# Kernel tuning notes

Measured on AMD Instinct MI355X. Metric: run time of the kernel, lower is better.

The kernel has to match this reference:

```python
import jax, jax.numpy as jnp
import numpy as np

PAD = 0
C_CONST = 0.1712209


def setup_inputs() -> dict:
    key = jax.random.key(0)
    ks = jax.random.split(key, 6)
    tlen, bsz, slen, hsize, vocab = 64, 32, 64, 1024, 32000
    hidden = jax.random.normal(ks[0], (tlen, bsz, hsize), dtype=jnp.float32)
    context = jax.random.normal(ks[1], (slen, bsz, hsize), dtype=jnp.float32)
    src = jax.random.randint(ks[2], (bsz, slen), 0, vocab, dtype=jnp.int64)
    stdv = 1.0 / np.sqrt(hsize)
    W_gen = jax.random.uniform(ks[3], (vocab, hsize), dtype=jnp.float32, minval=-stdv, maxval=stdv)
    b_gen = jnp.zeros((vocab,), dtype=jnp.float32)
    # Xavier-like init for the copy gate
    w_copy = jax.random.normal(ks[4], (hsize,), dtype=jnp.float32) * np.sqrt(2.0 / (hsize + 1))
    b_copy = jnp.zeros((1,), dtype=jnp.float32)
    return {"hidden": hidden, "context": context, "src": src,
            "W_gen": W_gen, "b_gen": b_gen, "w_copy": w_copy, "b_copy": b_copy}


def reference(hidden, context, src, W_gen, b_gen, w_copy, b_copy):
    tlen, bsz, hsize = hidden.shape
    # p(z=1): probability of copying, [tlen, bsz, 1]
    copy_prob = jax.nn.sigmoid(jnp.einsum('tbh,h->tb', hidden, w_copy) + b_copy[0])[..., None]
    # generator distribution over tgt vocab
    logits = jnp.einsum('tbh,vh->tbv', hidden, W_gen) + b_gen
    prob = jax.nn.softmax(logits.astype(jnp.float32), axis=-1)
    p_g = prob * (1.0 - copy_prob)  # [tlen, bsz, vocab]
    # copy attention over source positions: bmm(query[b,t,h], keys[b,s,h]^T)
    attn_score = jnp.einsum('tbh,sbh->bts', hidden, context)  # [bsz, tlen, slen]
    src_mask = (src == PAD)[:, None, :]  # [bsz, 1, slen]
    attn_score = jnp.where(src_mask, -jnp.inf, attn_score.astype(jnp.float32))
    attns = jax.nn.softmax(attn_score, axis=-1)  # [bsz, tlen, slen]
    p_c = jnp.transpose(attns, (1, 0, 2)) * copy_prob  # [tlen, bsz, slen]
    # scatter_add copy probs into vocab distribution along dim 2
    slen = src.shape[1]
    idx_src = jnp.broadcast_to(src[None, :, :], (tlen, bsz, slen))
    t_idx = jnp.arange(tlen)[:, None, None]
    b_idx = jnp.arange(bsz)[None, :, None]
    p_g = p_g.at[t_idx, b_idx, idx_src].add(p_c)
    return jnp.log(p_g) + C_CONST
```

## Files before the change

kernel.cpp:

```cpp
#include <hip/hip_runtime.h>
#include <hip/hip_bf16.h>
#include <stdint.h>

#define TLEN 64
#define BSZ 32
#define SLEN 64
#define HS 1024
#define VOC 32000
#define NROW (TLEN*BSZ)
#define C_CONST_F 0.1712209f
#define BK 64

typedef __attribute__((ext_vector_type(8))) short short8;
typedef __attribute__((ext_vector_type(4))) float f32x4;

static __device__ __forceinline__ ushort f2bf(float f) {
    uint32_t u = __builtin_bit_cast(uint32_t, f);
    uint32_t r = (u + 0x7fffu + ((u >> 16) & 1u)) >> 16;
    return (ushort)r;
}
static __device__ __forceinline__ float bf2f(ushort u) {
    uint32_t v = ((uint32_t)u) << 16;
    return __builtin_bit_cast(float, v);
}
static __device__ __forceinline__ void async16(const void* g, void* lds) {
    __builtin_amdgcn_global_load_lds(
        (const __attribute__((address_space(1))) void*)g,
        (__attribute__((address_space(3))) void*)lds, 16, 0, 0);
}
static __device__ __forceinline__ int swz12(int e) { return e ^ (((e >> 4) & 15) << 1); }

__global__ __launch_bounds__(256) void gate_kernel(const float* __restrict__ hidden,
                                                   const float* __restrict__ w_copy,
                                                   const float* __restrict__ b_copy,
                                                   float* __restrict__ cp) {
    int wid = threadIdx.x >> 6, lane = threadIdx.x & 63;
    int row = blockIdx.x * 4 + wid;
    const float* h = hidden + (size_t)row * HS;
    float acc = 0.f;
    for (int i = 0; i < 4; ++i) {
        int off = (i * 64 + lane) * 4;
        float4 a = *(const float4*)(h + off);
        float4 w = *(const float4*)(w_copy + off);
        acc += a.x * w.x + a.y * w.y + a.z * w.z + a.w * w.w;
    }
    for (int m = 32; m >= 1; m >>= 1) acc += __shfl_xor(acc, m, 64);
    if (lane == 0) cp[row] = 1.f / (1.f + expf(-(acc + b_copy[0])));
}

__global__ __launch_bounds__(256) void attn_kernel(const float* __restrict__ hidden,
                                                   const float* __restrict__ context,
                                                   const int* __restrict__ src,
                                                   const float* __restrict__ cp,
                                                   float* __restrict__ p_c) {
    int row = blockIdx.x;
    int b = row & (BSZ - 1);
    int tid = threadIdx.x, wid = tid >> 6, lane = tid & 63;
    __shared__ float hrow[HS];
    __shared__ float sc[SLEN];
    *(float4*)(hrow + tid * 4) = *(const float4*)(hidden + (size_t)row * HS + tid * 4);
    __syncthreads();
    for (int j = 0; j < 16; ++j) {
        int s = wid * 16 + j;
        const float* c = context + ((size_t)s * BSZ + b) * HS;
        float acc = 0.f;
        for (int i = 0; i < 4; ++i) {
            int off = (i * 64 + lane) * 4;
            float4 cv = *(const float4*)(c + off);
            float4 hv = *(const float4*)(hrow + off);
            acc += cv.x * hv.x + cv.y * hv.y + cv.z * hv.z + cv.w * hv.w;
        }
        for (int m = 32; m >= 1; m >>= 1) acc += __shfl_xor(acc, m, 64);
        if (lane == 0) sc[s] = acc;
    }
    __syncthreads();
    if (tid < SLEN) {
        float v = sc[tid];
        if (src[b * SLEN + tid] == 0) v = -INFINITY;
        float m = v;
        for (int k = 32; k >= 1; k >>= 1) m = fmaxf(m, __shfl_xor(m, k, 64));
        float e = expf(v - m);
        float ssum = e;
        for (int k = 32; k >= 1; k >>= 1) ssum += __shfl_xor(ssum, k, 64);
        p_c[row * SLEN + tid] = (e / ssum) * cp[row];
    }
}

__global__ __launch_bounds__(256) void cvt_kernel(const float* __restrict__ in,
                                                  ushort* __restrict__ out, int n4) {
    int i = blockIdx.x * blockDim.x + threadIdx.x;
    if (i >= n4) return;
    float4 v = ((const float4*)in)[i];
    ushort4 o;
    o.x = f2bf(v.x); o.y = f2bf(v.y); o.z = f2bf(v.z); o.w = f2bf(v.w);
    ((ushort4*)out)[i] = o;
}

template <bool BF16L>
__global__ __launch_bounds__(256) void gemm_kernel(const ushort* __restrict__ A,
                                                   const ushort* __restrict__ B,
                                                   const float* __restrict__ b_gen,
                                                   void* __restrict__ logits,
                                                   float* __restrict__ partials ) {
    __shared__ ushort sAB[2 * 128 * BK];
    ushort* sA = sAB;
    ushort* sB = sAB + 128 * BK;

    int orig = blockIdx.x;
    int wg = (orig & 7) * 500 + (orig >> 3);
    int mIdx = wg & 15;
    int nIdx = wg >> 4;
    int m0 = mIdx * 128, n0 = nIdx * 128;
    int tid = threadIdx.x, wid = tid >> 6, lane = tid & 63;
    int wm = (wid >> 1) * 64, wn = (wid & 1) * 64;
    int lr = lane & 15, lg = lane >> 4;

    const ushort* gaP[4]; const ushort* gbP[4]; char* laP[4]; char* lbP[4];
    for (int j = 0; j < 4; ++j) {
        int slot = j * 256 + tid;
        int row = slot >> 3;
        int cc = (slot & 7) ^ (row & 7);
        gaP[j] = A + (size_t)(m0 + row) * HS + cc * 8;
        gbP[j] = B + (size_t)(n0 + row) * HS + cc * 8;
        laP[j] = (char*)sA + (size_t)(j * 256 + wid * 64) * 16;
        lbP[j] = (char*)sB + (size_t)(j * 256 + wid * 64) * 16;
    }

    f32x4 acc[4][4];
    for (int m = 0; m < 4; ++m)
        for (int n = 0; n < 4; ++n)
            acc[m][n] = f32x4{0.f, 0.f, 0.f, 0.f};

    int offA[4][2], offB[4][2];
    for (int mb = 0; mb < 4; ++mb) {
        int row = wm + mb * 16 + lr;
        for (int kk = 0; kk < 2; ++kk)
            offA[mb][kk] = row * (BK * 2) + (((kk * 4 + lg) ^ (row & 7)) << 4);
    }
    for (int nb = 0; nb < 4; ++nb) {
        int row = wn + nb * 16 + lr;
        for (int kk = 0; kk < 2; ++kk)
            offB[nb][kk] = row * (BK * 2) + (((kk * 4 + lg) ^ (row & 7)) << 4);
    }

    for (int k0 = 0; k0 < HS; k0 += BK) {
        for (int j = 0; j < 4; ++j) {
            async16(gaP[j] + k0, laP[j]);
            async16(gbP[j] + k0, lbP[j]);
        }
        __syncthreads();
        for (int kk = 0; kk < 2; ++kk) {
            short8 af[4], bfr[4];
            for (int mb = 0; mb < 4; ++mb)
                af[mb] = *(const short8*)((const char*)sA + offA[mb][kk]);
            for (int nb = 0; nb < 4; ++nb)
                bfr[nb] = *(const short8*)((const char*)sB + offB[nb][kk]);
            for (int mb = 0; mb < 4; ++mb)
                for (int nb = 0; nb < 4; ++nb)
                    acc[mb][nb] = __builtin_amdgcn_mfma_f32_16x16x32_bf16(af[mb], bfr[nb], acc[mb][nb], 0, 0, 0);
        }
        __syncthreads();
    }

    float bg[4];
    for (int nb = 0; nb < 4; ++nb) bg[nb] = b_gen[n0 + wn + nb * 16 + lr];
    int chunk = nIdx * 2 + (wid & 1);
    ushort* stile = sAB + wid * 4096;

    for (int mb = 0; mb < 4; ++mb) {
        for (int r = 0; r < 4; ++r) {
            int rl = mb * 16 + lg * 4 + r;
            int row = m0 + wm + rl;
            float v[4];
            float mx = -INFINITY;
            for (int nb = 0; nb < 4; ++nb) {
                v[nb] = acc[mb][nb][r] + bg[nb];
                mx = fmaxf(mx, v[nb]);
            }
            if (BF16L) {
                for (int nb = 0; nb < 4; ++nb) {
                    int cl = nb * 16 + lr;
                    int slot_w = (cl >> 3) ^ (rl & 7);
                    stile[rl * 64 + slot_w * 8 + (cl & 7)] = f2bf(v[nb]);
                }
            } else {
                float* out = (float*)logits;
                for (int nb = 0; nb < 4; ++nb)
                    out[(size_t)row * VOC + n0 + wn + nb * 16 + lr] = v[nb];
            }
            for (int k = 8; k >= 1; k >>= 1) mx = fmaxf(mx, __shfl_xor(mx, k, 16));
            float se = 0.f;
            for (int nb = 0; nb < 4; ++nb) se += __expf(v[nb] - mx);
            for (int k = 8; k >= 1; k >>= 1) se += __shfl_xor(se, k, 16);
            if (lr == 0) {
                float2 pv; pv.x = mx; pv.y = se;
                *(float2*)(partials + ((size_t)row * 500 + chunk) * 2) = pv;
            }
        }
    }
    if (BF16L) {
        __syncthreads();
        ushort* Lbf = (ushort*)logits;
        for (int rep = 0; rep < 8; ++rep) {
            int rl = rep * 8 + (lane >> 3);
            int slot_r = (lane & 7) ^ (rl & 7);
            short8 val = *(const short8*)(stile + rl * 64 + slot_r * 8);
            ushort* dst = Lbf + (size_t)(m0 + wm + rl) * VOC + n0 + wn + (lane & 7) * 8;
            *(short8*)dst = val;
        }
    }
}

__global__ __launch_bounds__(256) void reduce_kernel(const float* __restrict__ partials,
                                                     float* __restrict__ Ms,
                                                     float* __restrict__ Ss) {
    int wid = threadIdx.x >> 6, lane = threadIdx.x & 63;
    int row = blockIdx.x * 4 + wid;
    float m = -INFINITY, s = 0.f;
    for (int c = lane; c < 500; c += 64) {
        float2 p = *(const float2*)(partials + ((size_t)row * 500 + c) * 2);
        float nm = fmaxf(m, p.x);
        s = s * __expf(m - nm) + p.y * __expf(p.x - nm);
        m = nm;
    }
    for (int k = 32; k >= 1; k >>= 1) {
        float om = __shfl_xor(m, k, 64), os = __shfl_xor(s, k, 64);
        float nm = fmaxf(m, om);
        s = s * __expf(m - nm) + os * __expf(om - nm);
        m = nm;
    }
    if (lane == 0) { Ms[row] = m; Ss[row] = s; }
}

template <bool BF16L>
__global__ __launch_bounds__(256) void finalize_kernel(const int* __restrict__ src,
                                                       const float* __restrict__ p_c,
                                                       const float* __restrict__ cp,
                                                       const float* __restrict__ Ms,
                                                       const float* __restrict__ Ss,
                                                       const void* __restrict__ logits,
                                                       float* __restrict__ out) {
    int row = blockIdx.y;
    int c0 = blockIdx.x * 4096;
    int b = row & (BSZ - 1);
    __shared__ float addv[4096];
    int tid = threadIdx.x;
    for (int i = tid; i < 4096; i += 256) addv[i] = 0.f;
    __syncthreads();
    if (tid < SLEN) {
        int v = src[b * SLEN + tid];
        if (v >= c0 && v < c0 + 4096)
            atomicAdd(&addv[swz12(v - c0)], p_c[row * SLEN + tid]);
    }
    __syncthreads();
    int col = c0 + tid * 16;
    if (col >= VOC) return;
    float M = Ms[row];
    float g = (1.f - cp[row]) / Ss[row];
    float L[16];
    if (BF16L) {
        const ushort* lb = (const ushort*)logits + (size_t)row * VOC + col;
        short8 a = *(const short8*)lb;
        short8 c = *(const short8*)(lb + 8);
        for (int i = 0; i < 8; ++i) { L[i] = bf2f((ushort)a[i]); L[8 + i] = bf2f((ushort)c[i]); }
    } else {
        const float* lf = (const float*)logits + (size_t)row * VOC + col;
        for (int i = 0; i < 4; ++i) {
            float4 v = *(const float4*)(lf + i * 4);
            L[i * 4 + 0] = v.x; L[i * 4 + 1] = v.y; L[i * 4 + 2] = v.z; L[i * 4 + 3] = v.w;
        }
    }
    float res[16];
    for (int i = 0; i < 16; ++i) {
        float p = __expf(L[i] - M) * g + addv[swz12(tid * 16 + i)];
        res[i] = __logf(p) + C_CONST_F;
    }
    float* op = out + (size_t)row * VOC + col;
    for (int i = 0; i < 4; ++i) {
        float4 v;
        v.x = res[i * 4 + 0]; v.y = res[i * 4 + 1]; v.z = res[i * 4 + 2]; v.w = res[i * 4 + 3];
        *(float4*)(op + i * 4) = v;
    }
}

extern "C" void kernel_launch(void* const* d_in, const int* in_sizes, int n_in,
                              void* d_out, int out_size, void* d_ws, size_t ws_size,
                              hipStream_t stream) {
    const float* hidden  = (const float*)d_in[0];
    const float* context = (const float*)d_in[1];
    const int*   src     = (const int*)d_in[2];
    const float* W_gen   = (const float*)d_in[3];
    const float* b_gen   = (const float*)d_in[4];
    const float* w_copy  = (const float*)d_in[5];
    const float* b_copy  = (const float*)d_in[6];
    float* out = (float*)d_out;
    char* ws = (char*)d_ws;

    float*  cp       = (float*)(ws);
    float*  p_c      = (float*)(ws + 8192);
    float*  Ms       = (float*)(ws + 532480);
    float*  Ss       = (float*)(ws + 540672);
    float*  partials = (float*)(ws + 548864);
    ushort* Abf      = (ushort*)(ws + 8740864);
    ushort* Wbf      = (ushort*)(ws + 12935168);
    ushort* Lbf      = (ushort*)(ws + 78471168);
    const size_t NEED_BF16 = 209543168;

    gate_kernel<<<NROW / 4, 256, 0, stream>>>(hidden, w_copy, b_copy, cp);
    attn_kernel<<<NROW, 256, 0, stream>>>(hidden, context, src, cp, p_c);
    cvt_kernel<<<(NROW * HS / 4) / 256, 256, 0, stream>>>(hidden, Abf, NROW * HS / 4);
    cvt_kernel<<<(VOC * HS / 4) / 256, 256, 0, stream>>>(W_gen, Wbf, VOC * HS / 4);

    dim3 fgrid(8, NROW);
    if (ws_size >= NEED_BF16) {
        gemm_kernel<true><<<(NROW / 128) * (VOC / 128), 256, 0, stream>>>(Abf, Wbf, b_gen, Lbf, partials);
        reduce_kernel<<<NROW / 4, 256, 0, stream>>>(partials, Ms, Ss);
        finalize_kernel<true><<<fgrid, 256, 0, stream>>>(src, p_c, cp, Ms, Ss, Lbf, out);
    } else {
        gemm_kernel<false><<<(NROW / 128) * (VOC / 128), 256, 0, stream>>>(Abf, Wbf, b_gen, out, partials);
        reduce_kernel<<<NROW / 4, 256, 0, stream>>>(partials, Ms, Ss);
        finalize_kernel<false><<<fgrid, 256, 0, stream>>>(src, p_c, cp, Ms, Ss, out, out);
    }
}
```

Measured before the change: 391.9 us.

## Enlarge GEMM tiles to 256x256 with a 4-slot async LDS pipeline

Rewrites the vocabulary-projection GEMM to use 256x256 output tiles across 8 waves (512 threads), with K split into 32-wide steps. A 4-slot LDS ring is kept three stages ahead using direct global-to-LDS loads, paced by explicit vmcnt waits and barriers, and MFMA issue is raised in priority. This aims to increase data reuse per loaded byte and to hide global-load latency behind compute, replacing the old load-then-sync loop. In exchange it uses 128KB of LDS and more accumulator registers per block, which limits occupancy, and the epilogue is reworked to fit the larger per-wave tiles.

```diff
diff --git a/kernel.cpp b/kernel.cpp
--- a/kernel.cpp
+++ b/kernel.cpp
@@ -9,7 +9,13 @@
 #define VOC 32000
 #define NROW (TLEN*BSZ)
 #define C_CONST_F 0.1712209f
-#define BK 64
+
+#define BM 256
+#define BN 256
+#define BKT 32
+#define NKT (HS/BKT)
+#define SLOT_BYTES 32768
+#define B_REGION 16384
 
 typedef __attribute__((ext_vector_type(8))) short short8;
 typedef __attribute__((ext_vector_type(4))) float f32x4;
@@ -97,99 +103,133 @@
 }
 
 template <bool BF16L>
-__global__ __launch_bounds__(256) void gemm_kernel(const ushort* __restrict__ A,
-                                                   const ushort* __restrict__ B,
-                                                   const float* __restrict__ b_gen,
-                                                   void* __restrict__ logits,
-                                                   float* __restrict__ partials ) {
-    __shared__ ushort sAB[2 * 128 * BK];
-    ushort* sA = sAB;
-    ushort* sB = sAB + 128 * BK;
+__global__ __launch_bounds__(512, 2) void gemm_kernel(const ushort* __restrict__ A,
+                                                      const ushort* __restrict__ B,
+                                                      const float* __restrict__ b_gen,
+                                                      void* __restrict__ logits,
+                                                      float* __restrict__ partials ) {
+    __shared__ ushort sAB[4 * SLOT_BYTES / 2];
 
     int orig = blockIdx.x;
-    int wg = (orig & 7) * 500 + (orig >> 3);
-    int mIdx = wg & 15;
-    int nIdx = wg >> 4;
-    int m0 = mIdx * 128, n0 = nIdx * 128;
+    int wg = (orig & 7) * 125 + (orig >> 3);
+    int mIdx = wg & 7;
+    int nIdx = wg >> 3;
+    int m0 = mIdx * BM, n0 = nIdx * BN;
     int tid = threadIdx.x, wid = tid >> 6, lane = tid & 63;
-    int wm = (wid >> 1) * 64, wn = (wid & 1) * 64;
+    int wm = (wid >> 2) * 128, wn = (wid & 3) * 64;
     int lr = lane & 15, lg = lane >> 4;
 
-    const ushort* gaP[4]; const ushort* gbP[4]; char* laP[4]; char* lbP[4];
-    for (int j = 0; j < 4; ++j) {
-        int slot = j * 256 + tid;
-        int row = slot >> 3;
-        int cc = (slot & 7) ^ (row & 7);
-        gaP[j] = A + (size_t)(m0 + row) * HS + cc * 8;
-        gbP[j] = B + (size_t)(n0 + row) * HS + cc * 8;
-        laP[j] = (char*)sA + (size_t)(j * 256 + wid * 64) * 16;
-        lbP[j] = (char*)sB + (size_t)(j * 256 + wid * 64) * 16;
-    }
-
-    f32x4 acc[4][4];
-    for (int m = 0; m < 4; ++m)
-        for (int n = 0; n < 4; ++n)
-            acc[m][n] = f32x4{0.f, 0.f, 0.f, 0.f};
-
-    int offA[4][2], offB[4][2];
-    for (int mb = 0; mb < 4; ++mb) {
-        int row = wm + mb * 16 + lr;
-        for (int kk = 0; kk < 2; ++kk)
-            offA[mb][kk] = row * (BK * 2) + (((kk * 4 + lg) ^ (row & 7)) << 4);
-    }
-    for (int nb = 0; nb < 4; ++nb) {
-        int row = wn + nb * 16 + lr;
-        for (int kk = 0; kk < 2; ++kk)
-            offB[nb][kk] = row * (BK * 2) + (((kk * 4 + lg) ^ (row & 7)) << 4);
-    }
-
-    for (int k0 = 0; k0 < HS; k0 += BK) {
-        for (int j = 0; j < 4; ++j) {
-            async16(gaP[j] + k0, laP[j]);
-            async16(gbP[j] + k0, lbP[j]);
-        }
-        __syncthreads();
-        for (int kk = 0; kk < 2; ++kk) {
-            short8 af[4], bfr[4];
-            for (int mb = 0; mb < 4; ++mb)
-                af[mb] = *(const short8*)((const char*)sA + offA[mb][kk]);
-            for (int nb = 0; nb < 4; ++nb)
-                bfr[nb] = *(const short8*)((const char*)sB + offB[nb][kk]);
-            for (int mb = 0; mb < 4; ++mb)
-                for (int nb = 0; nb < 4; ++nb)
-                    acc[mb][nb] = __builtin_amdgcn_mfma_f32_16x16x32_bf16(af[mb], bfr[nb], acc[mb][nb], 0, 0, 0);
-        }
-        __syncthreads();
-    }
+    const ushort* gA[2]; const ushort* gB[2];
+    uint32_t ldsOffA[2], ldsOffB[2];
+    #pragma unroll
+    for (int j = 0; j < 2; ++j) {
+        int s = j * 512 + tid;
+        int row = s >> 2;
+        int kc = (s & 3) ^ ((row >> 1) & 3);
+        gA[j] = A + (size_t)(m0 + row) * HS + kc * 8;
+        gB[j] = B + (size_t)(n0 + row) * HS + kc * 8;
+        ldsOffA[j] = (uint32_t)((j * 512 + wid * 64) * 16);
+        ldsOffB[j] = (uint32_t)(B_REGION + (j * 512 + wid * 64) * 16);
+    }
+
+    uint32_t kcs   = (uint32_t)((lg ^ ((lr >> 1) & 3)) * 16);
+    uint32_t offAb = (uint32_t)(wm + lr) * 64 + kcs;
+    uint32_t offBb = B_REGION + (uint32_t)(wn + lr) * 64 + kcs;
+
+    f32x4 acc[8][4];
+    #pragma unroll
+    for (int m = 0; m < 8; ++m)
+        #pragma unroll
+        for (int n = 0; n < 4; ++n) acc[m][n] = f32x4{0.f, 0.f, 0.f, 0.f};
+
+    for (int kt = 0; kt < 3; ++kt) {
+        char* sd = (char*)sAB + kt * SLOT_BYTES;
+        int k0 = kt * BKT;
+        #pragma unroll
+        for (int j = 0; j < 2; ++j) {
+            async16(gA[j] + k0, sd + ldsOffA[j]);
+            async16(gB[j] + k0, sd + ldsOffB[j]);
+        }
+    }
+
+#define PHASE_BODY(KT, DOSTAGE)                                                        \
+    {                                                                                  \
+        const char* sl = (const char*)sAB + ((KT) & 3) * SLOT_BYTES;                   \
+        short8 af[8], bv[4];                                                           \
+        _Pragma("unroll")                                                              \
+        for (int mb = 0; mb < 8; ++mb)                                                 \
+            af[mb] = *(const short8*)(sl + offAb + mb * 1024);                         \
+        _Pragma("unroll")                                                              \
+        for (int nb = 0; nb < 4; ++nb)                                                 \
+            bv[nb] = *(const short8*)(sl + offBb + nb * 1024);                         \
+        if (DOSTAGE) {                                                                 \
+            char* sd = (char*)sAB + (((KT) + 3) & 3) * SLOT_BYTES;                     \
+            int k0s = ((KT) + 3) * BKT;                                                \
+            _Pragma("unroll")                                                          \
+            for (int j = 0; j < 2; ++j) {                                              \
+                async16(gA[j] + k0s, sd + ldsOffA[j]);                                 \
+                async16(gB[j] + k0s, sd + ldsOffB[j]);                                 \
+            }                                                                          \
+        }                                                                              \
+        __builtin_amdgcn_s_setprio(1);                                                 \
+        _Pragma("unroll")                                                              \
+        for (int mb = 0; mb < 8; ++mb)                                                 \
+            _Pragma("unroll")                                                          \
+            for (int nb = 0; nb < 4; ++nb)                                             \
+                acc[mb][nb] = __builtin_amdgcn_mfma_f32_16x16x32_bf16(af[mb], bv[nb],  \
+                                                                     acc[mb][nb], 0, 0, 0); \
+        __builtin_amdgcn_s_setprio(0);                                                 \
+    }
+
+    for (int kt = 0; kt < NKT - 3; ++kt) {
+        asm volatile("s_waitcnt vmcnt(8)\n\ts_barrier" ::: "memory");
+        PHASE_BODY(kt, true);
+    }
+    asm volatile("s_waitcnt vmcnt(8)\n\ts_barrier" ::: "memory");
+    PHASE_BODY(NKT - 3, false);
+    asm volatile("s_waitcnt vmcnt(4)\n\ts_barrier" ::: "memory");
+    PHASE_BODY(NKT - 2, false);
+    asm volatile("s_waitcnt vmcnt(0)\n\ts_barrier" ::: "memory");
+    PHASE_BODY(NKT - 1, false);
+#undef PHASE_BODY
+
+    asm volatile("s_barrier" ::: "memory");
 
     float bg[4];
+    #pragma unroll
     for (int nb = 0; nb < 4; ++nb) bg[nb] = b_gen[n0 + wn + nb * 16 + lr];
-    int chunk = nIdx * 2 + (wid & 1);
-    ushort* stile = sAB + wid * 4096;
-
-    for (int mb = 0; mb < 4; ++mb) {
+    int chunk = nIdx * 4 + (wid & 3);
+    ushort* stile = sAB + wid * 8192;
+
+    #pragma unroll
+    for (int mb = 0; mb < 8; ++mb) {
+        #pragma unroll
         for (int r = 0; r < 4; ++r) {
             int rl = mb * 16 + lg * 4 + r;
             int row = m0 + wm + rl;
             float v[4];
             float mx = -INFINITY;
+            #pragma unroll
             for (int nb = 0; nb < 4; ++nb) {
                 v[nb] = acc[mb][nb][r] + bg[nb];
                 mx = fmaxf(mx, v[nb]);
             }
             if (BF16L) {
+                #pragma unroll
                 for (int nb = 0; nb < 4; ++nb) {
                     int cl = nb * 16 + lr;
                     int slot_w = (cl >> 3) ^ (rl & 7);
                     stile[rl * 64 + slot_w * 8 + (cl & 7)] = f2bf(v[nb]);
                 }
             } else {
-                float* out = (float*)logits;
+                float* outp = (float*)logits;
+                #pragma unroll
                 for (int nb = 0; nb < 4; ++nb)
-                    out[(size_t)row * VOC + n0 + wn + nb * 16 + lr] = v[nb];
+                    outp[(size_t)row * VOC + n0 + wn + nb * 16 + lr] = v[nb];
             }
             for (int k = 8; k >= 1; k >>= 1) mx = fmaxf(mx, __shfl_xor(mx, k, 16));
             float se = 0.f;
+            #pragma unroll
             for (int nb = 0; nb < 4; ++nb) se += __expf(v[nb] - mx);
             for (int k = 8; k >= 1; k >>= 1) se += __shfl_xor(se, k, 16);
             if (lr == 0) {
@@ -199,13 +239,14 @@
         }
     }
     if (BF16L) {
-        __syncthreads();
         ushort* Lbf = (ushort*)logits;
-        for (int rep = 0; rep < 8; ++rep) {
-            int rl = rep * 8 + (lane >> 3);
-            int slot_r = (lane & 7) ^ (rl & 7);
+        #pragma unroll
+        for (int rep = 0; rep < 16; ++rep) {
+            int idx = rep * 64 + lane;
+            int rl = idx >> 3, c8 = idx & 7;
+            int slot_r = c8 ^ (rl & 7);
             short8 val = *(const short8*)(stile + rl * 64 + slot_r * 8);
-            ushort* dst = Lbf + (size_t)(m0 + wm + rl) * VOC + n0 + wn + (lane & 7) * 8;
+            ushort* dst = Lbf + (size_t)(m0 + wm + rl) * VOC + n0 + wn + c8 * 8;
             *(short8*)dst = val;
         }
     }
@@ -311,13 +352,14 @@
     cvt_kernel<<<(NROW * HS / 4) / 256, 256, 0, stream>>>(hidden, Abf, NROW * HS / 4);
     cvt_kernel<<<(VOC * HS / 4) / 256, 256, 0, stream>>>(W_gen, Wbf, VOC * HS / 4);
 
+    int ggrid = (NROW / BM) * (VOC / BN);
     dim3 fgrid(8, NROW);
     if (ws_size >= NEED_BF16) {
-        gemm_kernel<true><<<(NROW / 128) * (VOC / 128), 256, 0, stream>>>(Abf, Wbf, b_gen, Lbf, partials);
+        gemm_kernel<true><<<ggrid, 512, 0, stream>>>(Abf, Wbf, b_gen, Lbf, partials);
         reduce_kernel<<<NROW / 4, 256, 0, stream>>>(partials, Ms, Ss);
         finalize_kernel<true><<<fgrid, 256, 0, stream>>>(src, p_c, cp, Ms, Ss, Lbf, out);
     } else {
-        gemm_kernel<false><<<(NROW / 128) * (VOC / 128), 256, 0, stream>>>(Abf, Wbf, b_gen, out, partials);
+        gemm_kernel<false><<<ggrid, 512, 0, stream>>>(Abf, Wbf, b_gen, out, partials);
         reduce_kernel<<<NROW / 4, 256, 0, stream>>>(partials, Ms, Ss);
         finalize_kernel<false><<<fgrid, 256, 0, stream>>>(src, p_c, cp, Ms, Ss, out, out);
     }
```

New measurement: 342.1 us. 12.7% less time.
